# Kernel optimization log

Hardware: AMD Instinct MI355X
Metric: run time of the kernel (lower is better)

The kernel has to match this reference:

```python
import jax, jax.numpy as jnp
import numpy as np

NUM_HEADS = 12

def setup_inputs() -> dict:
    key = jax.random.key(0)
    ks = jax.random.split(key, 8)
    B, N, C = 8, 1024, 768
    H = NUM_HEADS
    return {
        "x": jax.random.normal(ks[0], (B, N, C), dtype=jnp.float32),
        "relative_position_index": jax.random.randint(ks[1], (N, N), 0, 2048, dtype=jnp.int64),
        "qkv_weight": jax.random.normal(ks[2], (3 * C, C), dtype=jnp.float32) * 0.02,
        "q_bias": jax.random.normal(ks[3], (C,), dtype=jnp.float32) * 0.02,
        "v_bias": jax.random.normal(ks[4], (C,), dtype=jnp.float32) * 0.02,
        "proj_weight": jax.random.normal(ks[5], (C, C), dtype=jnp.float32) * 0.02,
        "proj_bias": jax.random.normal(ks[6], (C,), dtype=jnp.float32) * 0.02,
        "rel_pos_bias_table": jax.random.normal(ks[7], (2048, H), dtype=jnp.float32) * 0.02,
    }

def reference(x, relative_position_index, qkv_weight, q_bias, v_bias, proj_weight, proj_bias, rel_pos_bias_table):
    B, N, C = x.shape
    H = NUM_HEADS
    d = C // H
    scale = d ** (-0.5)
    # qkv bias: (q_bias, zeros, v_bias) as in the torch module
    qkv_b = jnp.concatenate([q_bias, jnp.zeros_like(v_bias), v_bias])
    qkv = x @ qkv_weight.T + qkv_b  # [B,N,3C]
    qkv = qkv.reshape(B, N, 3, H, d).transpose(2, 0, 3, 1, 4)  # [3,B,H,N,d]
    q, k, v = qkv[0], qkv[1], qkv[2]
    attn = jnp.einsum("bhnd,bhmd->bhnm", q * scale, k)  # [B,H,N,N]
    # relative position bias: table lookup [N,N,H] -> [H,N,N]
    bias = rel_pos_bias_table[relative_position_index].transpose(2, 0, 1)
    attn = attn + bias[None]
    attn = jax.nn.softmax(attn, axis=-1)
    out = jnp.einsum("bhnm,bhmd->bhnd", attn, v)  # [B,H,N,d]
    out = out.transpose(0, 2, 1, 3).reshape(B, N, C)
    return out @ proj_weight.T + proj_bias
```

## Files before the change

kernel.cpp:

```cpp
#include <hip/hip_runtime.h>

typedef unsigned short ushort_t;
typedef __bf16 bf16x8 __attribute__((ext_vector_type(8)));
typedef float f32x4 __attribute__((ext_vector_type(4)));

#define MFMA(a, b, c) __builtin_amdgcn_mfma_f32_16x16x32_bf16((a), (b), (c), 0, 0, 0)

#define BATCH 8
#define SEQ 1024
#define CDIM 768
#define NH 12
#define HD 64
#define MTOT (BATCH * SEQ)
#define THREEC (3 * CDIM)
#define KVB 64
#define LOG2E 1.44269504088896f

__device__ __forceinline__ ushort_t f2bf(float f) {
    unsigned int u = __builtin_bit_cast(unsigned int, f);
    u = (u + 0x7FFFu + ((u >> 16) & 1u)) >> 16;
    return (ushort_t)u;
}
__device__ __forceinline__ float bf2f(ushort_t b) {
    unsigned int u = ((unsigned int)b) << 16;
    return __builtin_bit_cast(float, u);
}
__device__ __forceinline__ ushort_t bfbits(float f) {
    __bf16 h = (__bf16)f;
    return __builtin_bit_cast(ushort_t, h);
}

typedef const __attribute__((address_space(1))) unsigned int* gas_ptr;
typedef __attribute__((address_space(3))) unsigned int* las_ptr;

__device__ __forceinline__ void async16(const ushort_t* g, ushort_t* l) {
    __builtin_amdgcn_global_load_lds((gas_ptr)(const void*)g, (las_ptr)(void*)l, 16, 0, 0);
}

#define WAITVM_(N) asm volatile("s_waitcnt vmcnt(" #N ")" ::: "memory")
#define WAITVM(N) WAITVM_(N)
#define SCHEDB __builtin_amdgcn_sched_barrier(0)

__global__ __launch_bounds__(256) void k_convert(const float* __restrict__ x,
                                                 const float* __restrict__ wq,
                                                 const float* __restrict__ wp,
                                                 ushort_t* __restrict__ xb,
                                                 ushort_t* __restrict__ wqb,
                                                 ushort_t* __restrict__ wpb) {
    const int NX = MTOT * CDIM / 4;
    const int NQ = THREEC * CDIM / 4;
    const int NP = CDIM * CDIM / 4;
    int i = blockIdx.x * 256 + threadIdx.x;
    const float4* src;
    ushort_t* dst;
    int off;
    if (i < NX) { src = (const float4*)x; dst = xb; off = i; }
    else if (i < NX + NQ) { src = (const float4*)wq; dst = wqb; off = i - NX; }
    else if (i < NX + NQ + NP) { src = (const float4*)wp; dst = wpb; off = i - NX - NQ; }
    else return;
    float4 v = src[off];
    ushort4 o;
    o.x = f2bf(v.x); o.y = f2bf(v.y); o.z = f2bf(v.z); o.w = f2bf(v.w);
    ((ushort4*)dst)[off] = o;
}

__global__ __launch_bounds__(256) void k_bias(const int* __restrict__ rpi,
                                              const float* __restrict__ table,
                                              ushort_t* __restrict__ biasF) {
    __shared__ int idx_s[16][64];
    int tr = blockIdx.x;
    int tcq = blockIdx.y;
    int t = threadIdx.x;
    {
        int r = t >> 4;
        int c4 = (t & 15) * 4;
        int4 v = *(const int4*)&rpi[(tr * 16 + r) * SEQ + tcq * 64 + c4];
        *(int4*)&idx_s[r][c4] = v;
    }
    __syncthreads();
    int j = t >> 6;
    int lane = t & 63;
    int lq = lane >> 4, l15 = lane & 15;
    int tc = tcq * 4 + j;
    int id[4];
#pragma unroll
    for (int rr = 0; rr < 4; rr++) id[rr] = idx_s[l15][j * 16 + lq * 4 + rr];
#pragma unroll
    for (int h = 0; h < NH; h++) {
        ushort4 o;
        o.x = f2bf(table[id[0] * NH + h] * LOG2E);
        o.y = f2bf(table[id[1] * NH + h] * LOG2E);
        o.z = f2bf(table[id[2] * NH + h] * LOG2E);
        o.w = f2bf(table[id[3] * NH + h] * LOG2E);
        *(ushort4*)&biasF[(((h * 64 + tr) * 64 + tc) * 256 + lane * 4)] = o;
    }
}

template <int MODE>
__global__ __launch_bounds__(256) void k_gemm(const ushort_t* __restrict__ A,
                                              const ushort_t* __restrict__ Bw,
                                              const float* __restrict__ biasq,
                                              const float* __restrict__ biasv,
                                              const float* __restrict__ biasp,
                                              ushort_t* __restrict__ qb,
                                              ushort_t* __restrict__ kb,
                                              ushort_t* __restrict__ vT,
                                              float* __restrict__ outp) {
    __shared__ __attribute__((aligned(16))) ushort_t As[128 * 64];
    __shared__ __attribute__((aligned(16))) ushort_t Bs[128 * 64];
    const int K = CDIM;
    int tid = threadIdx.x, wave = tid >> 6, lane = tid & 63;
    int l15 = lane & 15, lq = lane >> 4;
    int wm = wave >> 1, wn = wave & 1;
    int rowBase = blockIdx.y * 128;
    int colBase = blockIdx.x * 128;
    f32x4 acc[4][4] = {};
    int srow = wave * 8 + (lane >> 3);
    int scol = (((lane & 7) ^ (srow & 7))) * 8;
    int l7 = l15 & 7;
    for (int k0 = 0; k0 < K; k0 += 64) {
#pragma unroll
        for (int is = 0; is < 4; is++) {
            async16(A + (rowBase + is * 32 + srow) * K + k0 + scol,
                    As + is * 2048 + tid * 8);
            async16(Bw + (colBase + is * 32 + srow) * K + k0 + scol,
                    Bs + is * 2048 + tid * 8);
        }
        asm volatile("s_waitcnt vmcnt(0)" ::: "memory");
        __syncthreads();
#pragma unroll
        for (int kk = 0; kk < 64; kk += 32) {
            bf16x8 af[4], bfr[4];
#pragma unroll
            for (int mf = 0; mf < 4; mf++)
                af[mf] = *(const bf16x8*)&As[(wm * 64 + mf * 16 + l15) * 64 +
                                             ((((kk >> 3) + lq) ^ l7) * 8)];
#pragma unroll
            for (int nf = 0; nf < 4; nf++)
                bfr[nf] = *(const bf16x8*)&Bs[(wn * 64 + nf * 16 + l15) * 64 +
                                              ((((kk >> 3) + lq) ^ l7) * 8)];
#pragma unroll
            for (int mf = 0; mf < 4; mf++)
#pragma unroll
                for (int nf = 0; nf < 4; nf++)
                    acc[mf][nf] = MFMA(af[mf], bfr[nf], acc[mf][nf]);
        }
        __syncthreads();
    }
#pragma unroll
    for (int mf = 0; mf < 4; mf++) {
#pragma unroll
        for (int nf = 0; nf < 4; nf++) {
            int jc = colBase + wn * 64 + nf * 16 + l15;
            int mg0 = rowBase + wm * 64 + mf * 16 + (lane >> 4) * 4;
            if (MODE == 0) {
                int which = jc / CDIM;
                int co = jc - which * CDIM;
                int b = mg0 >> 10, tok0 = mg0 & 1023;
                int hh = co >> 6, dd = co & 63;
                int bh = b * NH + hh;
                if (which == 0) {
                    float bq_ = biasq[co];
#pragma unroll
                    for (int r = 0; r < 4; r++)
                        qb[(bh * SEQ + tok0 + r) * HD + dd] =
                            f2bf((acc[mf][nf][r] + bq_) * 0.125f);
                } else if (which == 1) {
#pragma unroll
                    for (int r = 0; r < 4; r++)
                        kb[(bh * SEQ + tok0 + r) * HD + dd] = f2bf(acc[mf][nf][r]);
                } else {
                    float bv = biasv[co];
                    ushort4 pk;
                    pk.x = f2bf(acc[mf][nf][0] + bv);
                    pk.y = f2bf(acc[mf][nf][1] + bv);
                    pk.z = f2bf(acc[mf][nf][2] + bv);
                    pk.w = f2bf(acc[mf][nf][3] + bv);
                    *(ushort4*)&vT[(size_t)(bh * HD + dd) * SEQ + tok0] = pk;
                }
            } else {
                float bp_ = biasp[jc];
#pragma unroll
                for (int r = 0; r < 4; r++)
                    outp[(size_t)(mg0 + r) * CDIM + jc] = acc[mf][nf][r] + bp_;
            }
        }
    }
}

__global__ __launch_bounds__(256, 3) void k_attn(const ushort_t* __restrict__ qb,
                                                 const ushort_t* __restrict__ kb,
                                                 const ushort_t* __restrict__ vT,
                                                 const ushort_t* __restrict__ biasF,
                                                 ushort_t* __restrict__ ctx) {
    __shared__ __attribute__((aligned(16))) ushort_t Ks[2][KVB * 64];
    __shared__ __attribute__((aligned(16))) ushort_t Vs[2][KVB * 64];
    __shared__ __attribute__((aligned(16))) ushort_t Ps[4][32][72];

    int bid = ((int)blockIdx.x & 7) * 96 + ((int)blockIdx.x >> 3);
    int qt = bid & 7;
    int bh = bid >> 3;
    int b = bh / NH, h = bh - b * NH;
    int tid = threadIdx.x, w = tid >> 6, lane = tid & 63;
    int l15 = lane & 15, lq = lane >> 4, lq4 = lq * 4;
    int row0 = qt * 128 + w * 32;
    int qtile0 = row0 >> 4;

    const ushort_t* qp = qb + bh * SEQ * HD;
    const ushort_t* kp = kb + bh * SEQ * HD;
    const ushort_t* vp = vT + bh * HD * SEQ;
    const ushort_t* bfp0 = biasF + (size_t)(h * 64 + qtile0) * 64 * 256;
    const ushort_t* bfp1 = bfp0 + 64 * 256;
    ushort_t* Pw = &Ps[w][0][0];

    int rk0, sk0, rk1, sk1;
    {
        int cid0 = tid;
        rk0 = cid0 >> 3; sk0 = ((cid0 & 7) ^ (rk0 & 7)) * 8;
        int cid1 = 256 + tid;
        rk1 = cid1 >> 3; sk1 = ((cid1 & 7) ^ (rk1 & 7)) * 8;
    }

#define STAGE_K(BUF, C0)                                                    \
    do {                                                                    \
        async16(kp + ((C0) + rk0) * HD + sk0, &Ks[BUF][tid * 8]);           \
        async16(kp + ((C0) + rk1) * HD + sk1, &Ks[BUF][(256 + tid) * 8]);   \
    } while (0)
#define STAGE_V(BUF, C0)                                                    \
    do {                                                                    \
        async16(vp + rk0 * SEQ + (C0) + sk0, &Vs[BUF][tid * 8]);            \
        async16(vp + rk1 * SEQ + (C0) + sk1, &Vs[BUF][(256 + tid) * 8]);    \
    } while (0)

    STAGE_K(0, 0); STAGE_V(0, 0); STAGE_K(1, KVB); STAGE_V(1, KVB);

    bf16x8 qfr00 = *(const bf16x8*)&qp[(row0 + l15) * HD + 8 * lq];
    bf16x8 qfr01 = *(const bf16x8*)&qp[(row0 + l15) * HD + 32 + 8 * lq];
    bf16x8 qfr10 = *(const bf16x8*)&qp[(row0 + 16 + l15) * HD + 8 * lq];
    bf16x8 qfr11 = *(const bf16x8*)&qp[(row0 + 16 + l15) * HD + 32 + 8 * lq];

    f32x4 Oa0[4] = {}, Oa1[4] = {};
    float mi0 = -1e30f, mi1 = -1e30f, li0 = 0.0f, li1 = 0.0f;
    f32x4 accA0[4], accA1[4], accB0[4], accB1[4];

#define QK_BLOCK(AN0, AN1, KN)                                                 \
    do {                                                                       \
        __builtin_amdgcn_s_setprio(1);                                         \
        _Pragma("unroll") for (int n = 0; n < 4; n++) {                        \
            int krow = n * 16 + l15;                                           \
            bf16x8 kf0 = *(const bf16x8*)&(KN)[krow * 64 + ((lq ^ (krow & 7)) * 8)]; \
            bf16x8 kf1 = *(const bf16x8*)&(KN)[krow * 64 + (((lq + 4) ^ (krow & 7)) * 8)]; \
            f32x4 z0 = {};                                                     \
            z0 = MFMA(kf0, qfr00, z0); z0 = MFMA(kf1, qfr01, z0);              \
            (AN0)[n] = z0;                                                     \
            f32x4 z1 = {};                                                     \
            z1 = MFMA(kf0, qfr10, z1); z1 = MFMA(kf1, qfr11, z1);              \
            (AN1)[n] = z1;                                                     \
        }                                                                      \
        __builtin_amdgcn_s_setprio(0);                                         \
    } while (0)

#define SOFTMAX_HALF(ACC, BFR, MI, LI, OA, ROWOFF)                             \
    do {                                                                       \
        f32x4 z[4];                                                            \
        _Pragma("unroll") for (int n = 0; n < 4; n++) {                        \
            z[n][0] = fmaf((ACC)[n][0], LOG2E, bf2f((BFR)[n].x));              \
            z[n][1] = fmaf((ACC)[n][1], LOG2E, bf2f((BFR)[n].y));              \
            z[n][2] = fmaf((ACC)[n][2], LOG2E, bf2f((BFR)[n].z));              \
            z[n][3] = fmaf((ACC)[n][3], LOG2E, bf2f((BFR)[n].w));              \
        }                                                                      \
        float tm;                                                              \
        {                                                                      \
            f32x4 mv;                                                          \
            _Pragma("unroll") for (int j = 0; j < 4; j++)                      \
                mv[j] = fmaxf(fmaxf(z[0][j], z[1][j]), fmaxf(z[2][j], z[3][j])); \
            tm = fmaxf(fmaxf(mv[0], mv[1]), fmaxf(mv[2], mv[3]));              \
        }                                                                      \
        tm = fmaxf(tm, __shfl_xor(tm, 16));                                    \
        tm = fmaxf(tm, __shfl_xor(tm, 32));                                    \
        if (!__all(tm <= (MI) + 8.0f)) {                                       \
            float mn = fmaxf((MI), tm);                                        \
            float al = exp2f((MI) - mn);                                       \
            (MI) = mn; (LI) *= al;                                             \
            _Pragma("unroll") for (int r = 0; r < 4; r++) {                    \
                float alr = __shfl(al, (lane & 48) | (lq4 + r));               \
                (OA)[0][r] *= alr; (OA)[1][r] *= alr;                          \
                (OA)[2][r] *= alr; (OA)[3][r] *= alr;                          \
            }                                                                  \
        }                                                                      \
        f32x4 sv = {};                                                         \
        _Pragma("unroll") for (int n = 0; n < 4; n++) {                        \
            z[n][0] = exp2f(z[n][0] - (MI)); z[n][1] = exp2f(z[n][1] - (MI));  \
            z[n][2] = exp2f(z[n][2] - (MI)); z[n][3] = exp2f(z[n][3] - (MI));  \
            sv += z[n];                                                        \
        }                                                                      \
        float s = (sv[0] + sv[1]) + (sv[2] + sv[3]);                           \
        s += __shfl_xor(s, 16);                                                \
        s += __shfl_xor(s, 32);                                                \
        (LI) += s;                                                             \
        _Pragma("unroll") for (int n = 0; n < 4; n++) {                        \
            ushort4 pk;                                                        \
            pk.x = bfbits(z[n][0]); pk.y = bfbits(z[n][1]);                    \
            pk.z = bfbits(z[n][2]); pk.w = bfbits(z[n][3]);                    \
            *(ushort4*)&Pw[((ROWOFF) + l15) * 72 + n * 16 + lq4] = pk;         \
        }                                                                      \
    } while (0)

#define PV_BLOCK(VC)                                                           \
    do {                                                                       \
        __builtin_amdgcn_s_setprio(1);                                         \
        _Pragma("unroll") for (int ks = 0; ks < 2; ks++) {                     \
            bf16x8 pf0 = *(const bf16x8*)&Pw[l15 * 72 + ks * 32 + lq * 8];     \
            bf16x8 pf1 = *(const bf16x8*)&Pw[(16 + l15) * 72 + ks * 32 + lq * 8]; \
            _Pragma("unroll") for (int nc = 0; nc < 4; nc++) {                 \
                int vrow = nc * 16 + l15;                                      \
                bf16x8 vf = *(const bf16x8*)&(VC)[vrow * 64 + (((ks * 4 + lq) ^ (vrow & 7)) * 8)]; \
                Oa0[nc] = MFMA(pf0, vf, Oa0[nc]);                              \
                Oa1[nc] = MFMA(pf1, vf, Oa1[nc]);                              \
            }                                                                  \
        }                                                                      \
        __builtin_amdgcn_s_setprio(0);                                         \
    } while (0)

#define ITER(T, AC0, AC1, AN0, AN1, DO_STAGE, DO_QK, VM)                       \
    do {                                                                       \
        WAITVM(VM);                                                            \
        SCHEDB;                                                                \
        __builtin_amdgcn_s_barrier();                                          \
        SCHEDB;                                                                \
        const int t_ = (T);                                                    \
        ushort4 bfr0[4], bfr1[4];                                              \
        {                                                                      \
            int kt0 = t_ * 4;                                                  \
            _Pragma("unroll") for (int n = 0; n < 4; n++) {                    \
                bfr0[n] = *(const ushort4*)&bfp0[(kt0 + n) * 256 + lane * 4];  \
                bfr1[n] = *(const ushort4*)&bfp1[(kt0 + n) * 256 + lane * 4];  \
            }                                                                  \
        }                                                                      \
        if (DO_STAGE) STAGE_K(t_ & 1, (t_ + 2) * KVB);                         \
        if (DO_QK) QK_BLOCK(AN0, AN1, Ks[(t_ + 1) & 1]);                       \
        SOFTMAX_HALF(AC0, bfr0, mi0, li0, Oa0, 0);                             \
        SOFTMAX_HALF(AC1, bfr1, mi1, li1, Oa1, 16);                            \
        PV_BLOCK(Vs[t_ & 1]);                                                  \
        if (DO_STAGE) {                                                        \
            SCHEDB;                                                            \
            __builtin_amdgcn_s_barrier();                                      \
            SCHEDB;                                                            \
            STAGE_V(t_ & 1, (t_ + 2) * KVB);                                   \
        }                                                                      \
    } while (0)

    WAITVM(6);
    SCHEDB;
    __builtin_amdgcn_s_barrier();
    SCHEDB;
    QK_BLOCK(accA0, accA1, Ks[0]);

#pragma unroll 1
    for (int tt = 0; tt < 14; tt += 2) {
        ITER(tt,     accA0, accA1, accB0, accB1, 1, 1, 2);
        ITER(tt + 1, accB0, accB1, accA0, accA1, 1, 1, 2);
    }
    ITER(14, accA0, accA1, accB0, accB1, 0, 1, 2);
    ITER(15, accB0, accB1, accA0, accA1, 0, 0, 0);

    float rli0 = 1.0f / li0, rli1 = 1.0f / li1;
#pragma unroll
    for (int r = 0; r < 4; r++) {
        float rl0 = __shfl(rli0, (lane & 48) | (lq4 + r));
        float rl1 = __shfl(rli1, (lane & 48) | (lq4 + r));
#pragma unroll
        for (int nc = 0; nc < 4; nc++) {
            ctx[(size_t)(b * SEQ + row0 + lq4 + r) * CDIM + h * HD + nc * 16 + l15] =
                bfbits(Oa0[nc][r] * rl0);
            ctx[(size_t)(b * SEQ + row0 + 16 + lq4 + r) * CDIM + h * HD + nc * 16 + l15] =
                bfbits(Oa1[nc][r] * rl1);
        }
    }
#undef ITER
#undef PV_BLOCK
#undef SOFTMAX_HALF
#undef QK_BLOCK
#undef STAGE_V
#undef STAGE_K
}

extern "C" void kernel_launch(void* const* d_in, const int* in_sizes, int n_in,
                              void* d_out, int out_size, void* d_ws, size_t ws_size,
                              hipStream_t stream) {
    const float* x = (const float*)d_in[0];
    const int* rpi = (const int*)d_in[1];
    const float* wqkv = (const float*)d_in[2];
    const float* qbias = (const float*)d_in[3];
    const float* vbias = (const float*)d_in[4];
    const float* wproj = (const float*)d_in[5];
    const float* pbias = (const float*)d_in[6];
    const float* table = (const float*)d_in[7];
    float* out = (float*)d_out;

    char* ws = (char*)d_ws;
    ushort_t* xb    = (ushort_t*)(ws + 0);
    ushort_t* wqb   = (ushort_t*)(ws + 12582912);
    ushort_t* wpb   = (ushort_t*)(ws + 16121856);
    ushort_t* qbuf  = (ushort_t*)(ws + 17301504);
    ushort_t* kbuf  = (ushort_t*)(ws + 29884416);
    ushort_t* vTbuf = (ushort_t*)(ws + 42467328);
    ushort_t* ctx   = (ushort_t*)(ws + 55050240);
    ushort_t* biasF = (ushort_t*)(ws + 67633152);

    k_convert<<<8448, 256, 0, stream>>>(x, wqkv, wproj, xb, wqb, wpb);
    k_bias<<<dim3(64, 16), 256, 0, stream>>>(rpi, table, biasF);
    k_gemm<0><<<dim3(THREEC / 128, MTOT / 128), 256, 0, stream>>>(
        xb, wqb, qbias, vbias, nullptr, qbuf, kbuf, vTbuf, nullptr);
    k_attn<<<768, 256, 0, stream>>>(qbuf, kbuf, vTbuf, biasF, ctx);
    k_gemm<1><<<dim3(CDIM / 128, MTOT / 128), 256, 0, stream>>>(
        ctx, wpb, nullptr, nullptr, pbias, nullptr, nullptr, nullptr, out);
}
```

Measured before the change: 181.2 us.

## Load V fragments directly from global into registers, drop V shared staging

The attention kernel stops staging V tiles through shared memory with async copies and instead has each lane load its V MFMA fragments straight from global memory into registers every iteration. This removes the V LDS buffers and the second barrier per iteration, and the launch bound goes from 3 to 4 blocks per CU to use the freed LDS for occupancy. In exchange, every wave fetches V redundantly from global/L2 with waitcnt forced to zero each iteration, which may expose global latency and raise register pressure.

```diff
diff --git a/kernel.cpp b/kernel.cpp
--- a/kernel.cpp
+++ b/kernel.cpp
@@ -188,13 +188,12 @@
     }
 }
 
-__global__ __launch_bounds__(256, 3) void k_attn(const ushort_t* __restrict__ qb,
+__global__ __launch_bounds__(256, 4) void k_attn(const ushort_t* __restrict__ qb,
                                                  const ushort_t* __restrict__ kb,
                                                  const ushort_t* __restrict__ vT,
                                                  const ushort_t* __restrict__ biasF,
                                                  ushort_t* __restrict__ ctx) {
     __shared__ __attribute__((aligned(16))) ushort_t Ks[2][KVB * 64];
-    __shared__ __attribute__((aligned(16))) ushort_t Vs[2][KVB * 64];
     __shared__ __attribute__((aligned(16))) ushort_t Ps[4][32][72];
 
     int bid = ((int)blockIdx.x & 7) * 96 + ((int)blockIdx.x >> 3);
@@ -226,18 +225,14 @@
         async16(kp + ((C0) + rk0) * HD + sk0, &Ks[BUF][tid * 8]);           \
         async16(kp + ((C0) + rk1) * HD + sk1, &Ks[BUF][(256 + tid) * 8]);   \
     } while (0)
-#define STAGE_V(BUF, C0)                                                    \
-    do {                                                                    \
-        async16(vp + rk0 * SEQ + (C0) + sk0, &Vs[BUF][tid * 8]);            \
-        async16(vp + rk1 * SEQ + (C0) + sk1, &Vs[BUF][(256 + tid) * 8]);    \
-    } while (0)
-
-    STAGE_K(0, 0); STAGE_V(0, 0); STAGE_K(1, KVB); STAGE_V(1, KVB);
 
     bf16x8 qfr00 = *(const bf16x8*)&qp[(row0 + l15) * HD + 8 * lq];
     bf16x8 qfr01 = *(const bf16x8*)&qp[(row0 + l15) * HD + 32 + 8 * lq];
     bf16x8 qfr10 = *(const bf16x8*)&qp[(row0 + 16 + l15) * HD + 8 * lq];
     bf16x8 qfr11 = *(const bf16x8*)&qp[(row0 + 16 + l15) * HD + 32 + 8 * lq];
+
+    STAGE_K(0, 0);
+    STAGE_K(1, KVB);
 
     f32x4 Oa0[4] = {}, Oa1[4] = {};
     float mi0 = -1e30f, mi1 = -1e30f, li0 = 0.0f, li1 = 0.0f;
@@ -306,29 +301,14 @@
         }                                                                      \
     } while (0)
 
-#define PV_BLOCK(VC)                                                           \
+#define ITER(T, AC0, AC1, AN0, AN1, DO_STAGE, DO_QK)                           \
     do {                                                                       \
-        __builtin_amdgcn_s_setprio(1);                                         \
-        _Pragma("unroll") for (int ks = 0; ks < 2; ks++) {                     \
-            bf16x8 pf0 = *(const bf16x8*)&Pw[l15 * 72 + ks * 32 + lq * 8];     \
-            bf16x8 pf1 = *(const bf16x8*)&Pw[(16 + l15) * 72 + ks * 32 + lq * 8]; \
-            _Pragma("unroll") for (int nc = 0; nc < 4; nc++) {                 \
-                int vrow = nc * 16 + l15;                                      \
-                bf16x8 vf = *(const bf16x8*)&(VC)[vrow * 64 + (((ks * 4 + lq) ^ (vrow & 7)) * 8)]; \
-                Oa0[nc] = MFMA(pf0, vf, Oa0[nc]);                              \
-                Oa1[nc] = MFMA(pf1, vf, Oa1[nc]);                              \
-            }                                                                  \
-        }                                                                      \
-        __builtin_amdgcn_s_setprio(0);                                         \
-    } while (0)
-
-#define ITER(T, AC0, AC1, AN0, AN1, DO_STAGE, DO_QK, VM)                       \
-    do {                                                                       \
-        WAITVM(VM);                                                            \
+        WAITVM(0);                                                             \
         SCHEDB;                                                                \
         __builtin_amdgcn_s_barrier();                                          \
         SCHEDB;                                                                \
         const int t_ = (T);                                                    \
+                       \
         ushort4 bfr0[4], bfr1[4];                                              \
         {                                                                      \
             int kt0 = t_ * 4;                                                  \
@@ -337,20 +317,29 @@
                 bfr1[n] = *(const ushort4*)&bfp1[(kt0 + n) * 256 + lane * 4];  \
             }                                                                  \
         }                                                                      \
+                      \
+        bf16x8 vr[2][4];                                                       \
+        _Pragma("unroll") for (int ks = 0; ks < 2; ks++)                       \
+            _Pragma("unroll") for (int nc = 0; nc < 4; nc++)                   \
+                vr[ks][nc] = *(const bf16x8*)&vp[(nc * 16 + l15) * SEQ +       \
+                                                 t_ * KVB + ks * 32 + lq * 8]; \
         if (DO_STAGE) STAGE_K(t_ & 1, (t_ + 2) * KVB);                         \
         if (DO_QK) QK_BLOCK(AN0, AN1, Ks[(t_ + 1) & 1]);                       \
         SOFTMAX_HALF(AC0, bfr0, mi0, li0, Oa0, 0);                             \
         SOFTMAX_HALF(AC1, bfr1, mi1, li1, Oa1, 16);                            \
-        PV_BLOCK(Vs[t_ & 1]);                                                  \
-        if (DO_STAGE) {                                                        \
-            SCHEDB;                                                            \
-            __builtin_amdgcn_s_barrier();                                      \
-            SCHEDB;                                                            \
-            STAGE_V(t_ & 1, (t_ + 2) * KVB);                                   \
-        }                                                                      \
+        __builtin_amdgcn_s_setprio(1);                                         \
+        _Pragma("unroll") for (int ks = 0; ks < 2; ks++) {                     \
+            bf16x8 pf0 = *(const bf16x8*)&Pw[l15 * 72 + ks * 32 + lq * 8];     \
+            bf16x8 pf1 = *(const bf16x8*)&Pw[(16 + l15) * 72 + ks * 32 + lq * 8]; \
+            _Pragma("unroll") for (int nc = 0; nc < 4; nc++) {                 \
+                Oa0[nc] = MFMA(pf0, vr[ks][nc], Oa0[nc]);                      \
+                Oa1[nc] = MFMA(pf1, vr[ks][nc], Oa1[nc]);                      \
+            }                                                                  \
+        }                                                                      \
+        __builtin_amdgcn_s_setprio(0);                                         \
     } while (0)
 
-    WAITVM(6);
+    WAITVM(2);
     SCHEDB;
     __builtin_amdgcn_s_barrier();
     SCHEDB;
@@ -358,11 +347,11 @@
 
 #pragma unroll 1
     for (int tt = 0; tt < 14; tt += 2) {
-        ITER(tt,     accA0, accA1, accB0, accB1, 1, 1, 2);
-        ITER(tt + 1, accB0, accB1, accA0, accA1, 1, 1, 2);
-    }
-    ITER(14, accA0, accA1, accB0, accB1, 0, 1, 2);
-    ITER(15, accB0, accB1, accA0, accA1, 0, 0, 0);
+        ITER(tt,     accA0, accA1, accB0, accB1, (tt < 14), 1);
+        ITER(tt + 1, accB0, accB1, accA0, accA1, (tt + 1 < 14), 1);
+    }
+    ITER(14, accA0, accA1, accB0, accB1, 0, 1);
+    ITER(15, accB0, accB1, accA0, accA1, 0, 0);
 
     float rli0 = 1.0f / li0, rli1 = 1.0f / li1;
 #pragma unroll
@@ -378,10 +367,8 @@
         }
     }
 #undef ITER
-#undef PV_BLOCK
 #undef SOFTMAX_HALF
 #undef QK_BLOCK
-#undef STAGE_V
 #undef STAGE_K
 }
 
```

Result: slower. 439.4 us (+142.5%).

## Build P operand via cross-lane shuffles instead of LDS round trip in attention

Applied to the files above, without the earlier changes.

Removes the per-wave shared-memory staging buffer for softmax probabilities. Packed bf16 probabilities are redistributed across lanes with shuffles to form the MFMA A-operand directly. It also remaps block indices so blocks sharing a head are grouped, and changes the per-iteration wait to full vmcnt(0). This avoids LDS write/read traffic and frees LDS for occupancy, but adds many shuffle instructions, and the stricter wait may expose load latency.

```diff
diff --git a/kernel.cpp b/kernel.cpp
--- a/kernel.cpp
+++ b/kernel.cpp
@@ -3,6 +3,7 @@
 typedef unsigned short ushort_t;
 typedef __bf16 bf16x8 __attribute__((ext_vector_type(8)));
 typedef float f32x4 __attribute__((ext_vector_type(4)));
+typedef unsigned int u32x4 __attribute__((ext_vector_type(4)));
 
 #define MFMA(a, b, c) __builtin_amdgcn_mfma_f32_16x16x32_bf16((a), (b), (c), 0, 0, 0)
 
@@ -28,6 +29,12 @@
 __device__ __forceinline__ ushort_t bfbits(float f) {
     __bf16 h = (__bf16)f;
     return __builtin_bit_cast(ushort_t, h);
+}
+__device__ __forceinline__ unsigned int pack2bf(float a, float b) {
+    ushort2 p;
+    p.x = bfbits(a);
+    p.y = bfbits(b);
+    return __builtin_bit_cast(unsigned int, p);
 }
 
 typedef const __attribute__((address_space(1))) unsigned int* gas_ptr;
@@ -195,12 +202,12 @@
                                                  ushort_t* __restrict__ ctx) {
     __shared__ __attribute__((aligned(16))) ushort_t Ks[2][KVB * 64];
     __shared__ __attribute__((aligned(16))) ushort_t Vs[2][KVB * 64];
-    __shared__ __attribute__((aligned(16))) ushort_t Ps[4][32][72];
-
-    int bid = ((int)blockIdx.x & 7) * 96 + ((int)blockIdx.x >> 3);
-    int qt = bid & 7;
-    int bh = bid >> 3;
-    int b = bh / NH, h = bh - b * NH;
+
+    int lin = ((int)blockIdx.x & 7) * 96 + ((int)blockIdx.x >> 3);
+    int h = lin >> 6;
+    int b = (lin >> 3) & 7;
+    int qt = lin & 7;
+    int bh = b * NH + h;
     int tid = threadIdx.x, w = tid >> 6, lane = tid & 63;
     int l15 = lane & 15, lq = lane >> 4, lq4 = lq * 4;
     int row0 = qt * 128 + w * 32;
@@ -211,7 +218,9 @@
     const ushort_t* vp = vT + bh * HD * SEQ;
     const ushort_t* bfp0 = biasF + (size_t)(h * 64 + qtile0) * 64 * 256;
     const ushort_t* bfp1 = bfp0 + 64 * 256;
-    ushort_t* Pw = &Ps[w][0][0];
+
+    int lamA = l15 + 32 * (lq & 1);
+    int lamB = lamA + 16;
 
     int rk0, sk0, rk1, sk1;
     {
@@ -242,6 +251,7 @@
     f32x4 Oa0[4] = {}, Oa1[4] = {};
     float mi0 = -1e30f, mi1 = -1e30f, li0 = 0.0f, li1 = 0.0f;
     f32x4 accA0[4], accA1[4], accB0[4], accB1[4];
+    unsigned int u0[4][2], u1[4][2];
 
 #define QK_BLOCK(AN0, AN1, KN)                                                 \
     do {                                                                       \
@@ -260,7 +270,7 @@
         __builtin_amdgcn_s_setprio(0);                                         \
     } while (0)
 
-#define SOFTMAX_HALF(ACC, BFR, MI, LI, OA, ROWOFF)                             \
+#define SOFTMAX_HALF(ACC, BFR, MI, LI, OA, UH)                                 \
     do {                                                                       \
         f32x4 z[4];                                                            \
         _Pragma("unroll") for (int n = 0; n < 4; n++) {                        \
@@ -299,32 +309,48 @@
         s += __shfl_xor(s, 32);                                                \
         (LI) += s;                                                             \
         _Pragma("unroll") for (int n = 0; n < 4; n++) {                        \
-            ushort4 pk;                                                        \
-            pk.x = bfbits(z[n][0]); pk.y = bfbits(z[n][1]);                    \
-            pk.z = bfbits(z[n][2]); pk.w = bfbits(z[n][3]);                    \
-            *(ushort4*)&Pw[((ROWOFF) + l15) * 72 + n * 16 + lq4] = pk;         \
-        }                                                                      \
+            (UH)[n][0] = pack2bf(z[n][0], z[n][1]);                            \
+            (UH)[n][1] = pack2bf(z[n][2], z[n][3]);                            \
+        }                                                                      \
+    } while (0)
+
+#define ASSEMBLE(UH, KS, PF)                                                   \
+    do {                                                                       \
+        unsigned int a0 = __shfl((int)(UH)[2 * (KS)][0], lamA);                \
+        unsigned int b0 = __shfl((int)(UH)[2 * (KS) + 1][0], lamA);            \
+        unsigned int a1 = __shfl((int)(UH)[2 * (KS)][1], lamA);                \
+        unsigned int b1 = __shfl((int)(UH)[2 * (KS) + 1][1], lamA);            \
+        unsigned int a2 = __shfl((int)(UH)[2 * (KS)][0], lamB);                \
+        unsigned int b2 = __shfl((int)(UH)[2 * (KS) + 1][0], lamB);            \
+        unsigned int a3 = __shfl((int)(UH)[2 * (KS)][1], lamB);                \
+        unsigned int b3 = __shfl((int)(UH)[2 * (KS) + 1][1], lamB);            \
+        bool hi_ = (lq & 2) != 0;                                              \
+        u32x4 qd;                                                              \
+        qd[0] = hi_ ? b0 : a0; qd[1] = hi_ ? b1 : a1;                          \
+        qd[2] = hi_ ? b2 : a2; qd[3] = hi_ ? b3 : a3;                          \
+        (PF) = __builtin_bit_cast(bf16x8, qd);                                 \
     } while (0)
 
 #define PV_BLOCK(VC)                                                           \
     do {                                                                       \
         __builtin_amdgcn_s_setprio(1);                                         \
         _Pragma("unroll") for (int ks = 0; ks < 2; ks++) {                     \
-            bf16x8 pf0 = *(const bf16x8*)&Pw[l15 * 72 + ks * 32 + lq * 8];     \
-            bf16x8 pf1 = *(const bf16x8*)&Pw[(16 + l15) * 72 + ks * 32 + lq * 8]; \
+            bf16x8 pfa, pfb;                                                   \
+            ASSEMBLE(u0, ks, pfa);                                             \
+            ASSEMBLE(u1, ks, pfb);                                             \
             _Pragma("unroll") for (int nc = 0; nc < 4; nc++) {                 \
                 int vrow = nc * 16 + l15;                                      \
                 bf16x8 vf = *(const bf16x8*)&(VC)[vrow * 64 + (((ks * 4 + lq) ^ (vrow & 7)) * 8)]; \
-                Oa0[nc] = MFMA(pf0, vf, Oa0[nc]);                              \
-                Oa1[nc] = MFMA(pf1, vf, Oa1[nc]);                              \
+                Oa0[nc] = MFMA(pfa, vf, Oa0[nc]);                              \
+                Oa1[nc] = MFMA(pfb, vf, Oa1[nc]);                              \
             }                                                                  \
         }                                                                      \
         __builtin_amdgcn_s_setprio(0);                                         \
     } while (0)
 
-#define ITER(T, AC0, AC1, AN0, AN1, DO_STAGE, DO_QK, VM)                       \
+#define ITER(T, AC0, AC1, AN0, AN1, DO_STAGE, DO_QK)                           \
     do {                                                                       \
-        WAITVM(VM);                                                            \
+        WAITVM(0);                                                             \
         SCHEDB;                                                                \
         __builtin_amdgcn_s_barrier();                                          \
         SCHEDB;                                                                \
@@ -339,8 +365,8 @@
         }                                                                      \
         if (DO_STAGE) STAGE_K(t_ & 1, (t_ + 2) * KVB);                         \
         if (DO_QK) QK_BLOCK(AN0, AN1, Ks[(t_ + 1) & 1]);                       \
-        SOFTMAX_HALF(AC0, bfr0, mi0, li0, Oa0, 0);                             \
-        SOFTMAX_HALF(AC1, bfr1, mi1, li1, Oa1, 16);                            \
+        SOFTMAX_HALF(AC0, bfr0, mi0, li0, Oa0, u0);                            \
+        SOFTMAX_HALF(AC1, bfr1, mi1, li1, Oa1, u1);                            \
         PV_BLOCK(Vs[t_ & 1]);                                                  \
         if (DO_STAGE) {                                                        \
             SCHEDB;                                                            \
@@ -358,11 +384,11 @@
 
 #pragma unroll 1
     for (int tt = 0; tt < 14; tt += 2) {
-        ITER(tt,     accA0, accA1, accB0, accB1, 1, 1, 2);
-        ITER(tt + 1, accB0, accB1, accA0, accA1, 1, 1, 2);
-    }
-    ITER(14, accA0, accA1, accB0, accB1, 0, 1, 2);
-    ITER(15, accB0, accB1, accA0, accA1, 0, 0, 0);
+        ITER(tt,     accA0, accA1, accB0, accB1, 1, 1);
+        ITER(tt + 1, accB0, accB1, accA0, accA1, 1, 1);
+    }
+    ITER(14, accA0, accA1, accB0, accB1, 0, 1);
+    ITER(15, accB0, accB1, accA0, accA1, 0, 0);
 
     float rli0 = 1.0f / li0, rli1 = 1.0f / li1;
 #pragma unroll
@@ -379,6 +405,7 @@
     }
 #undef ITER
 #undef PV_BLOCK
+#undef ASSEMBLE
 #undef SOFTMAX_HALF
 #undef QK_BLOCK
 #undef STAGE_V
```

Measured after the change: 178.7 us. About the same (-1.4%).
